# Optimization experiments

Hardware: AMD Instinct MI355X
Metric: run time of the kernel (lower is better)

## Reference

```python
import jax, jax.numpy as jnp
import numpy as np

N, T, D = 128, 2048, 88

def setup_inputs() -> dict:
    key = jax.random.key(0)
    k1, k2 = jax.random.split(key)
    output = jax.random.normal(k1, (N, T, D), dtype=jnp.float32)
    # binary piano-roll style target (sparse note activations)
    target = (jax.random.uniform(k2, (N, T, D)) < 0.1).astype(jnp.float32)
    mask = jnp.ones((N, T), dtype=jnp.int32)  # left-aligned valid mask
    return {"output": output, "target": target, "mask": mask}

def reference(output, target, mask):
    # prediction = (sigmoid(output) > 0.5) -> non-differentiable 0/1 floats
    pred = (jax.nn.sigmoid(output) > 0.5).astype(output.dtype)
    # tru_pos summed over both feature and time dims -> [N]
    tru_pos = jnp.sum(pred * target, axis=(1, 2))
    # per-timestep false pos / false neg -> [N, T]
    false_pos = jnp.sum(pred * (1.0 - target), axis=2)
    false_neg = jnp.sum((1.0 - pred) * target, axis=2)
    # T_i = number of valid timesteps per sequence (loop runs over t < T_i)
    T_i = jnp.sum(mask, axis=1)  # [N] int
    valid = (jnp.arange(false_pos.shape[1])[None, :] < T_i[:, None]).astype(output.dtype)
    ratio = tru_pos[:, None] / (tru_pos[:, None] + false_pos + false_neg)  # [N, T]
    acc = jnp.sum(ratio * valid, axis=1) / T_i.astype(output.dtype)  # [N]
    return jnp.sum(acc)
```

## Files before the change

kernel.cpp:

```cpp
#include <hip/hip_runtime.h>

#define NN 128
#define TT 2048
#define DD 88
#define ROWS_PER_BLK 128
#define F4_PER_ROW 22
#define F4_PER_TILE (ROWS_PER_BLK * F4_PER_ROW)
#define K1_BLOCKS (NN * TT / ROWS_PER_BLK)

__global__ __launch_bounds__(256) void acc_rowstats_kernel(
    const float* __restrict__ out, const float* __restrict__ tgt,
    float* __restrict__ fpfn, float* __restrict__ tp_part) {
  __shared__ float lds_x[F4_PER_TILE];
  const int tid = threadIdx.x;
  const int blk = blockIdx.x;
  const size_t tile_f4 = (size_t)blk * F4_PER_TILE;
  const float4* __restrict__ o4 = (const float4*)out;
  const float4* __restrict__ g4 = (const float4*)tgt;

  float tp = 0.f;
#pragma unroll
  for (int it = 0; it < 11; ++it) {
    const int f = it * 256 + tid;
    const float4 o = o4[tile_f4 + f];
    const float4 g = g4[tile_f4 + f];
    float x = 0.f;
    {
      const float pf = (o.x > 0.f) ? 1.f : 0.f;
      x += fabsf(pf - g.x);
      tp = fmaf(pf, g.x, tp);
    }
    {
      const float pf = (o.y > 0.f) ? 1.f : 0.f;
      x += fabsf(pf - g.y);
      tp = fmaf(pf, g.y, tp);
    }
    {
      const float pf = (o.z > 0.f) ? 1.f : 0.f;
      x += fabsf(pf - g.z);
      tp = fmaf(pf, g.z, tp);
    }
    {
      const float pf = (o.w > 0.f) ? 1.f : 0.f;
      x += fabsf(pf - g.w);
      tp = fmaf(pf, g.w, tp);
    }
    lds_x[f] = x;
  }
  __syncthreads();

  {
    const int r = tid >> 1;
    const int s = tid & 1;
    float v = 0.f;
#pragma unroll
    for (int i = 0; i < 11; ++i) v += lds_x[r * F4_PER_ROW + s * 11 + i];
    v += __shfl_down(v, 1, 64);
    if (s == 0) fpfn[(size_t)blk * ROWS_PER_BLK + r] = v;
  }

  for (int off = 32; off > 0; off >>= 1) tp += __shfl_down(tp, off, 64);
  __shared__ float s_tp[4];
  const int lane = tid & 63, wave = tid >> 6;
  if (lane == 0) s_tp[wave] = tp;
  __syncthreads();
  if (tid == 0) tp_part[blk] = s_tp[0] + s_tp[1] + s_tp[2] + s_tp[3];
}

__global__ __launch_bounds__(256) void acc_finalize_kernel(
    const int* __restrict__ mask, const float* __restrict__ fpfn,
    const float* __restrict__ tp_part, float* __restrict__ out) {
  const int n = blockIdx.x;
  const int tid = threadIdx.x;
  __shared__ float sa[256], sb[256];

  const int4* m4 = (const int4*)(mask + (size_t)n * TT);
  int ti = 0;
#pragma unroll
  for (int it = 0; it < 2; ++it) {
    const int4 v = m4[it * 256 + tid];
    ti += v.x + v.y + v.z + v.w;
  }
  const float tpv = (tid < 16) ? tp_part[n * 16 + tid] : 0.f;

  sa[tid] = (float)ti;
  sb[tid] = tpv;
  __syncthreads();
  for (int s = 128; s > 0; s >>= 1) {
    if (tid < s) { sa[tid] += sa[tid + s]; sb[tid] += sb[tid + s]; }
    __syncthreads();
  }
  const float fTi = sa[0];
  const float tp = sb[0];
  const int Ti = (int)fTi;
  __syncthreads();

  const float* __restrict__ fr = fpfn + (size_t)n * TT;
  float acc = 0.f;
  for (int t = tid; t < Ti; t += 256) acc += tp / (tp + fr[t]);
  sa[tid] = acc;
  __syncthreads();
  for (int s = 128; s > 0; s >>= 1) {
    if (tid < s) sa[tid] += sa[tid + s];
    __syncthreads();
  }
  if (tid == 0) atomicAdd(out, sa[0] / fTi);
}

extern "C" void kernel_launch(void* const* d_in, const int* in_sizes, int n_in,
                              void* d_out, int out_size, void* d_ws, size_t ws_size,
                              hipStream_t stream) {
  const float* output = (const float*)d_in[0];
  const float* target = (const float*)d_in[1];
  const int* mask = (const int*)d_in[2];
  float* out = (float*)d_out;

  float* tp_part = (float*)d_ws;
  float* fpfn = tp_part + K1_BLOCKS;

  hipMemsetAsync(d_out, 0, sizeof(float) * out_size, stream);
  acc_rowstats_kernel<<<K1_BLOCKS, 256, 0, stream>>>(output, target, fpfn, tp_part);
  acc_finalize_kernel<<<NN, 256, 0, stream>>>(mask, fpfn, tp_part, out);
}
```

Before: 208.3 us.

## Fuse row-stats and finalize kernels using atomic ticket last-block reduction

Merges the two kernels into one. The last block for each sequence, found through an atomic ticket counter, computes that sequence's accuracy, and a second ticket picks the final block to sum all sequences into the output. Per-sequence true positives are now accumulated with float atomics instead of partial arrays. This removes a kernel launch and the inter-kernel gap, at the cost of threadfences, atomics and a tail where single blocks do the serial finalize work.

```diff
diff --git a/kernel.cpp b/kernel.cpp
--- a/kernel.cpp
+++ b/kernel.cpp
@@ -6,24 +6,44 @@
 #define ROWS_PER_BLK 128
 #define F4_PER_ROW 22
 #define F4_PER_TILE (ROWS_PER_BLK * F4_PER_ROW)
-#define K1_BLOCKS (NN * TT / ROWS_PER_BLK)
+#define BLKS_PER_N (TT / ROWS_PER_BLK)
+#define GRID (NN * BLKS_PER_N)
 
-__global__ __launch_bounds__(256) void acc_rowstats_kernel(
+typedef float f4 __attribute__((ext_vector_type(4)));
+
+#define TP_OFF 0
+#define TICKET_OFF 128
+#define TICKET2_OFF 256
+#define ACC_OFF 260
+#define FPFN_OFF 512
+
+__global__ __launch_bounds__(256) void acc_fused_kernel(
     const float* __restrict__ out, const float* __restrict__ tgt,
-    float* __restrict__ fpfn, float* __restrict__ tp_part) {
+    const int* __restrict__ mask, float* __restrict__ ws,
+    float* __restrict__ outp) {
   __shared__ float lds_x[F4_PER_TILE];
+  __shared__ float s_tp[4];
+  __shared__ unsigned int s_old, s_old2;
+
+  float* tp_total = ws + TP_OFF;
+  unsigned int* ticket = (unsigned int*)(ws + TICKET_OFF);
+  unsigned int* ticket2 = (unsigned int*)(ws + TICKET2_OFF);
+  float* acc = ws + ACC_OFF;
+  float* fpfn = ws + FPFN_OFF;
+
   const int tid = threadIdx.x;
   const int blk = blockIdx.x;
+  const int n = blk / BLKS_PER_N;
   const size_t tile_f4 = (size_t)blk * F4_PER_TILE;
-  const float4* __restrict__ o4 = (const float4*)out;
-  const float4* __restrict__ g4 = (const float4*)tgt;
+  const f4* __restrict__ o4 = (const f4*)out;
+  const f4* __restrict__ g4 = (const f4*)tgt;
 
   float tp = 0.f;
 #pragma unroll
   for (int it = 0; it < 11; ++it) {
     const int f = it * 256 + tid;
-    const float4 o = o4[tile_f4 + f];
-    const float4 g = g4[tile_f4 + f];
+    const f4 o = o4[tile_f4 + f];
+    const f4 g = g4[tile_f4 + f];
     float x = 0.f;
     {
       const float pf = (o.x > 0.f) ? 1.f : 0.f;
@@ -60,19 +80,18 @@
   }
 
   for (int off = 32; off > 0; off >>= 1) tp += __shfl_down(tp, off, 64);
-  __shared__ float s_tp[4];
   const int lane = tid & 63, wave = tid >> 6;
   if (lane == 0) s_tp[wave] = tp;
   __syncthreads();
-  if (tid == 0) tp_part[blk] = s_tp[0] + s_tp[1] + s_tp[2] + s_tp[3];
-}
+  if (tid == 0) atomicAdd(&tp_total[n], s_tp[0] + s_tp[1] + s_tp[2] + s_tp[3]);
 
-__global__ __launch_bounds__(256) void acc_finalize_kernel(
-    const int* __restrict__ mask, const float* __restrict__ fpfn,
-    const float* __restrict__ tp_part, float* __restrict__ out) {
-  const int n = blockIdx.x;
-  const int tid = threadIdx.x;
-  __shared__ float sa[256], sb[256];
+  __threadfence();
+  if (tid == 0) s_old = atomicAdd(&ticket[n], 1u);
+  __syncthreads();
+  if (s_old != (unsigned)(BLKS_PER_N - 1)) return;
+
+  __threadfence();
+  float* sred = lds_x;
 
   const int4* m4 = (const int4*)(mask + (size_t)n * TT);
   int ti = 0;
@@ -81,30 +100,42 @@
     const int4 v = m4[it * 256 + tid];
     ti += v.x + v.y + v.z + v.w;
   }
-  const float tpv = (tid < 16) ? tp_part[n * 16 + tid] : 0.f;
-
-  sa[tid] = (float)ti;
-  sb[tid] = tpv;
+  sred[tid] = (float)ti;
   __syncthreads();
   for (int s = 128; s > 0; s >>= 1) {
-    if (tid < s) { sa[tid] += sa[tid + s]; sb[tid] += sb[tid + s]; }
+    if (tid < s) sred[tid] += sred[tid + s];
     __syncthreads();
   }
-  const float fTi = sa[0];
-  const float tp = sb[0];
+  const float fTi = sred[0];
   const int Ti = (int)fTi;
+  const float tpn = tp_total[n];
   __syncthreads();
 
   const float* __restrict__ fr = fpfn + (size_t)n * TT;
-  float acc = 0.f;
-  for (int t = tid; t < Ti; t += 256) acc += tp / (tp + fr[t]);
-  sa[tid] = acc;
+  float a = 0.f;
+  for (int t = tid; t < Ti; t += 256) a += tpn / (tpn + fr[t]);
+  sred[tid] = a;
   __syncthreads();
   for (int s = 128; s > 0; s >>= 1) {
-    if (tid < s) sa[tid] += sa[tid + s];
+    if (tid < s) sred[tid] += sred[tid + s];
     __syncthreads();
   }
-  if (tid == 0) atomicAdd(out, sa[0] / fTi);
+  if (tid == 0) {
+    acc[n] = sred[0] / fTi;
+    __threadfence();
+    s_old2 = atomicAdd(ticket2, 1u);
+  }
+  __syncthreads();
+  if (s_old2 != (unsigned)(NN - 1)) return;
+
+  __threadfence();
+  sred[tid] = (tid < NN) ? acc[tid] : 0.f;
+  __syncthreads();
+  for (int s = 128; s > 0; s >>= 1) {
+    if (tid < s) sred[tid] += sred[tid + s];
+    __syncthreads();
+  }
+  if (tid == 0) outp[0] = sred[0];
 }
 
 extern "C" void kernel_launch(void* const* d_in, const int* in_sizes, int n_in,
@@ -114,11 +145,8 @@
   const float* target = (const float*)d_in[1];
   const int* mask = (const int*)d_in[2];
   float* out = (float*)d_out;
+  float* ws = (float*)d_ws;
 
-  float* tp_part = (float*)d_ws;
-  float* fpfn = tp_part + K1_BLOCKS;
-
-  hipMemsetAsync(d_out, 0, sizeof(float) * out_size, stream);
-  acc_rowstats_kernel<<<K1_BLOCKS, 256, 0, stream>>>(output, target, fpfn, tp_part);
-  acc_finalize_kernel<<<NN, 256, 0, stream>>>(mask, fpfn, tp_part, out);
+  hipMemsetAsync(d_ws, 0, 512 * sizeof(float), stream);
+  acc_fused_kernel<<<GRID, 256, 0, stream>>>(output, target, mask, ws, out);
 }
```

After: 719.4 us. 245% more time.

## Stage tiles via direct global-to-LDS loads with smaller 32-row blocks

Applied to the files above, without the earlier changes.

Shrinks each block to 32 rows and loads the output and target tiles straight into LDS with the global_load_lds builtin, 16 bytes per lane, bypassing registers. Compute then reads from LDS, with 8 threads per row and a shuffle reduction. The aim is more blocks in flight and async bulk transfer for this memory-bound pass. The cost is four times as many partial TP values and LDS round trips for all input data; the finalize kernel is updated to read 64 partials per sequence.

```diff
diff --git a/kernel.cpp b/kernel.cpp
--- a/kernel.cpp
+++ b/kernel.cpp
@@ -1,67 +1,81 @@
 #include <hip/hip_runtime.h>
+#include <stdint.h>
 
 #define NN 128
 #define TT 2048
 #define DD 88
-#define ROWS_PER_BLK 128
-#define F4_PER_ROW 22
-#define F4_PER_TILE (ROWS_PER_BLK * F4_PER_ROW)
-#define K1_BLOCKS (NN * TT / ROWS_PER_BLK)
+#define ROWS 32
+#define F4_ROW 22
+#define F4_TILE (ROWS * F4_ROW)
+#define INSTR_PER_ARR 11
+#define K1_BLOCKS (NN * TT / ROWS)
+#define PARTS_PER_N (TT / ROWS)
+
+typedef float f4 __attribute__((ext_vector_type(4)));
+typedef const __attribute__((address_space(1))) uint32_t guint;
+typedef __attribute__((address_space(3))) uint32_t luint;
 
 __global__ __launch_bounds__(256) void acc_rowstats_kernel(
-    const float* __restrict__ out, const float* __restrict__ tgt,
+    const float* __restrict__ outp, const float* __restrict__ tgt,
     float* __restrict__ fpfn, float* __restrict__ tp_part) {
-  __shared__ float lds_x[F4_PER_TILE];
+  __shared__ f4 lds_o[F4_TILE];
+  __shared__ f4 lds_g[F4_TILE];
+  __shared__ float s_tp[4];
+
   const int tid = threadIdx.x;
+  const int lane = tid & 63;
+  const int wave = tid >> 6;
   const int blk = blockIdx.x;
-  const size_t tile_f4 = (size_t)blk * F4_PER_TILE;
-  const float4* __restrict__ o4 = (const float4*)out;
-  const float4* __restrict__ g4 = (const float4*)tgt;
+  const size_t tile_f = (size_t)blk * (ROWS * DD);
 
-  float tp = 0.f;
-#pragma unroll
-  for (int it = 0; it < 11; ++it) {
-    const int f = it * 256 + tid;
-    const float4 o = o4[tile_f4 + f];
-    const float4 g = g4[tile_f4 + f];
-    float x = 0.f;
-    {
-      const float pf = (o.x > 0.f) ? 1.f : 0.f;
-      x += fabsf(pf - g.x);
-      tp = fmaf(pf, g.x, tp);
-    }
-    {
-      const float pf = (o.y > 0.f) ? 1.f : 0.f;
-      x += fabsf(pf - g.y);
-      tp = fmaf(pf, g.y, tp);
-    }
-    {
-      const float pf = (o.z > 0.f) ? 1.f : 0.f;
-      x += fabsf(pf - g.z);
-      tp = fmaf(pf, g.z, tp);
-    }
-    {
-      const float pf = (o.w > 0.f) ? 1.f : 0.f;
-      x += fabsf(pf - g.w);
-      tp = fmaf(pf, g.w, tp);
-    }
-    lds_x[f] = x;
+  for (int j = wave; j < 2 * INSTR_PER_ARR; j += 4) {
+    const int is_g = (j >= INSTR_PER_ARR) ? 1 : 0;
+    const int idx = j - is_g * INSTR_PER_ARR;
+    const float* src = (is_g ? tgt : outp) + tile_f + idx * 256;
+    float* dst = (is_g ? (float*)lds_g : (float*)lds_o) + idx * 256;
+    __builtin_amdgcn_global_load_lds((guint*)src + lane * 4, (luint*)dst,
+                                     16, 0, 0);
   }
   __syncthreads();
 
-  {
-    const int r = tid >> 1;
-    const int s = tid & 1;
-    float v = 0.f;
+  const int r = tid >> 3;
+  const int s = tid & 7;
+  float tp = 0.f;
+  float x = 0.f;
 #pragma unroll
-    for (int i = 0; i < 11; ++i) v += lds_x[r * F4_PER_ROW + s * 11 + i];
-    v += __shfl_down(v, 1, 64);
-    if (s == 0) fpfn[(size_t)blk * ROWS_PER_BLK + r] = v;
+  for (int j0 = 0; j0 < 3; ++j0) {
+    const int j = s + j0 * 8;
+    if (j < F4_ROW) {
+      const f4 o = lds_o[r * F4_ROW + j];
+      const f4 g = lds_g[r * F4_ROW + j];
+      {
+        const float pf = (o.x > 0.f) ? 1.f : 0.f;
+        x += fabsf(pf - g.x);
+        tp = fmaf(pf, g.x, tp);
+      }
+      {
+        const float pf = (o.y > 0.f) ? 1.f : 0.f;
+        x += fabsf(pf - g.y);
+        tp = fmaf(pf, g.y, tp);
+      }
+      {
+        const float pf = (o.z > 0.f) ? 1.f : 0.f;
+        x += fabsf(pf - g.z);
+        tp = fmaf(pf, g.z, tp);
+      }
+      {
+        const float pf = (o.w > 0.f) ? 1.f : 0.f;
+        x += fabsf(pf - g.w);
+        tp = fmaf(pf, g.w, tp);
+      }
+    }
   }
+  x += __shfl_down(x, 4, 64);
+  x += __shfl_down(x, 2, 64);
+  x += __shfl_down(x, 1, 64);
+  if (s == 0) fpfn[(size_t)blk * ROWS + r] = x;
 
   for (int off = 32; off > 0; off >>= 1) tp += __shfl_down(tp, off, 64);
-  __shared__ float s_tp[4];
-  const int lane = tid & 63, wave = tid >> 6;
   if (lane == 0) s_tp[wave] = tp;
   __syncthreads();
   if (tid == 0) tp_part[blk] = s_tp[0] + s_tp[1] + s_tp[2] + s_tp[3];
@@ -81,7 +95,7 @@
     const int4 v = m4[it * 256 + tid];
     ti += v.x + v.y + v.z + v.w;
   }
-  const float tpv = (tid < 16) ? tp_part[n * 16 + tid] : 0.f;
+  const float tpv = (tid < PARTS_PER_N) ? tp_part[n * PARTS_PER_N + tid] : 0.f;
 
   sa[tid] = (float)ti;
   sb[tid] = tpv;
@@ -96,9 +110,9 @@
   __syncthreads();
 
   const float* __restrict__ fr = fpfn + (size_t)n * TT;
-  float acc = 0.f;
-  for (int t = tid; t < Ti; t += 256) acc += tp / (tp + fr[t]);
-  sa[tid] = acc;
+  float a = 0.f;
+  for (int t = tid; t < Ti; t += 256) a += tp / (tp + fr[t]);
+  sa[tid] = a;
   __syncthreads();
   for (int s = 128; s > 0; s >>= 1) {
     if (tid < s) sa[tid] += sa[tid + s];
```

Result: faster. 202.5 us, median of 2 (-2.8%).
